# Kernel optimization log

Hardware: AMD Instinct MI355X
Metric: run time of the kernel (lower is better)

Reference implementation:

```python
import jax, jax.numpy as jnp
import numpy as np
from jax import lax

B, N, M, K = 8, 8192, 2000, 16       # batch, raw pts, subsampled pts, neighbors
C1, C2, OUT = 128, 256, 100          # backbone widths, output_embed_size


def _fps(coords, m):
    """Farthest point sampling. coords [B,N,3] -> indices [B,m] (int32)."""
    b, n, _ = coords.shape
    init_last = jnp.zeros((b,), jnp.int32)

    def body(carry, _):
        mind, last = carry
        p = jnp.take_along_axis(coords, last[:, None, None], axis=1)  # [b,1,3]
        d = jnp.sum((coords - p) ** 2, axis=-1)                        # [b,n]
        mind = jnp.minimum(mind, d)
        nxt = jnp.argmax(mind, axis=-1).astype(jnp.int32)
        return (mind, nxt), nxt

    init = (jnp.full((b, n), 1e30, coords.dtype), init_last)
    _, rest = lax.scan(body, init, None, length=m - 1)                 # [m-1,b]
    return jnp.concatenate([init_last[None], rest], axis=0).T          # [b,m]


def _gather(src, idx):
    # src [B,N,C], idx [B,...] -> [B,...,C]
    return jax.vmap(lambda s, i: s[i])(src, idx)


def _knn(q, src, k):
    # squared-distance via |q|^2+|s|^2-2q.s to avoid a [B,M,N,3] intermediate
    d2 = (jnp.sum(q * q, -1)[:, :, None]
          + jnp.sum(src * src, -1)[:, None, :]
          - 2.0 * jnp.einsum('bmd,bnd->bmn', q, src))
    return lax.top_k(-d2, k)[1]                                        # [B,M,k]


def setup_inputs() -> dict:
    key = jax.random.key(0)
    ks = jax.random.split(key, 3)
    x = jax.random.uniform(ks[0], (B, N, 3), jnp.float32)
    W1 = jax.random.normal(ks[1], (6, C1), jnp.float32) * 0.1
    b1 = jnp.zeros((C1,), jnp.float32)
    W2 = jax.random.normal(ks[2], (3 + C1, C2), jnp.float32) * 0.1
    b2 = jnp.zeros((C2,), jnp.float32)
    return {"x": x, "W1": W1, "b1": b1, "W2": W2, "b2": b2}


def reference(x, W1, b1, W2, b2):
    coords = x
    cg = lax.stop_gradient(coords)          # indices are non-differentiable
    fps_idx = _fps(cg, M)                   # [B,M]
    sub = _gather(coords, fps_idx)          # [B,M,3]
    sub_g = lax.stop_gradient(sub)

    # --- point-conv layer 1: neighbors among raw points, feats = coords ---
    idx1 = _knn(sub_g, cg, K)               # [B,M,K]
    ngh = _gather(coords, idx1)             # [B,M,K,3]
    rel1 = ngh - sub[:, :, None, :]
    h1 = jax.nn.relu(jnp.einsum('bmkf,fc->bmkc',
                                jnp.concatenate([rel1, ngh], -1), W1) + b1)
    f1 = jnp.max(h1, axis=2)                # [B,M,C1]

    # --- point-conv layer 2: neighbors among subsampled points ---
    idx2 = _knn(sub_g, sub_g, K)            # [B,M,K]
    ngh2 = _gather(sub, idx2)               # [B,M,K,3]
    rel2 = ngh2 - sub[:, :, None, :]
    fg = _gather(f1, idx2)                  # [B,M,K,C1]
    h2 = jax.nn.relu(jnp.einsum('bmkf,fc->bmkc',
                                jnp.concatenate([rel2, fg], -1), W2) + b2)
    f2 = jnp.max(h2, axis=2)                # [B,M,C2]

    # --- fused adaptive max+avg pool: M % OUT == 0 -> uniform windows ---
    feat = jnp.transpose(f2, (0, 2, 1))     # [B,C2,M]
    windows = feat.reshape(B, C2, OUT, M // OUT)
    return jnp.max(windows, axis=-1) + jnp.mean(windows, axis=-1)  # [B,C2,OUT]
```

## Files before the change

### kernel.cpp

```cpp
#include <hip/hip_runtime.h>

#define B_    8
#define N_    8192
#define M_    2000
#define K_    16
#define C1_   128
#define C2_   256
#define OUT_  100
#define SUBP_ 2048

#define FPS_T 512
#define FPS_P 16

__device__ __forceinline__ unsigned long long umax64(unsigned long long a, unsigned long long b) {
    return a > b ? a : b;
}

template<int CTRL>
__device__ __forceinline__ unsigned long long dpp_max_u64(unsigned long long v) {
    int lo = __builtin_amdgcn_update_dpp(0, (int)(unsigned)(v & 0xFFFFFFFFull), CTRL, 0xF, 0xF, true);
    int hi = __builtin_amdgcn_update_dpp(0, (int)(v >> 32),                     CTRL, 0xF, 0xF, true);
    unsigned long long o = ((unsigned long long)(unsigned)hi << 32) | (unsigned)lo;
    return umax64(v, o);
}

template<int CTRL>
__device__ __forceinline__ float dpp_min_f32(float v) {
    int o = __builtin_amdgcn_update_dpp(__float_as_int(v), __float_as_int(v), CTRL, 0xF, 0xF, false);
    return fminf(v, __int_as_float(o));
}

__device__ __forceinline__ int spread3(int v) {
    return (v & 1) | ((v & 2) << 2) | ((v & 4) << 4);
}

__global__ __launch_bounds__(FPS_T, 1) void fps_kernel(const float* __restrict__ x,
                                                       float4* __restrict__ coords4,
                                                       float4* __restrict__ sub4) {
    int b = blockIdx.x;
    int t = threadIdx.x;
    int w = t >> 6, lane = t & 63;
    const float* X = x + (size_t)b * N_ * 3;
    float4* C4 = coords4 + b * N_;

    __shared__ float4 Clds[N_];
    __shared__ unsigned short sidx[N_];
    __shared__ unsigned int hist[512];
    __shared__ __align__(16) unsigned long long wkey[2][8];

    if (t < 512) hist[t] = 0u;
    if (t < SUBP_ - M_)
        sub4[b*SUBP_ + M_ + t] = make_float4(1e15f, 1e15f, 1e15f, 3e30f);
    __syncthreads();

    int cellv[FPS_P];
#pragma unroll
    for (int j = 0; j < FPS_P; ++j) {
        int i = t + j*FPS_T;
        float xx = X[i*3+0], yy = X[i*3+1], zz = X[i*3+2];
        float ss = fmaf(zz, zz, fmaf(yy, yy, xx*xx));
        float4 p = make_float4(xx, yy, zz, ss);
        C4[i] = p;
        Clds[i] = p;
        int cx = (int)(p.x * 8.0f); cx = cx < 0 ? 0 : (cx > 7 ? 7 : cx);
        int cy = (int)(p.y * 8.0f); cy = cy < 0 ? 0 : (cy > 7 ? 7 : cy);
        int cz = (int)(p.z * 8.0f); cz = cz < 0 ? 0 : (cz > 7 ? 7 : cz);
        int cell = (spread3(cx) << 2) | (spread3(cy) << 1) | spread3(cz);
        cellv[j] = cell;
        atomicAdd(&hist[cell], 1u);
    }
    __syncthreads();

    if (w == 0) {
        unsigned loc[8], tot = 0u;
#pragma unroll
        for (int c2 = 0; c2 < 8; ++c2) { loc[c2] = hist[lane*8 + c2]; tot += loc[c2]; }
        unsigned pre = tot;
#pragma unroll
        for (int d = 1; d < 64; d <<= 1) {
            unsigned o = __shfl_up(pre, d, 64);
            if (lane >= (unsigned)d) pre += o;
        }
        unsigned run = pre - tot;
#pragma unroll
        for (int c2 = 0; c2 < 8; ++c2) { unsigned v = loc[c2]; hist[lane*8 + c2] = run; run += v; }
    }
    __syncthreads();

#pragma unroll
    for (int j = 0; j < FPS_P; ++j) {
        int i = t + j*FPS_T;
        unsigned pos = atomicAdd(&hist[cellv[j]], 1u);
        sidx[pos] = (unsigned short)i;
    }
    __syncthreads();

    int oct = (w < 4) ? w : 11 - w;
    int sbase = oct*1024 + lane*FPS_P;
    float px_[FPS_P], py_[FPS_P], pz_[FPS_P], mind[FPS_P];
    unsigned inv_[FPS_P];
    float wx0 =  1e30f, wy0 =  1e30f, wz0 =  1e30f;
    float wx1 = -1e30f, wy1 = -1e30f, wz1 = -1e30f;
#pragma unroll
    for (int j = 0; j < FPS_P; ++j) {
        int o = (int)sidx[sbase + j];
        float4 p = Clds[o];
        px_[j] = p.x; py_[j] = p.y; pz_[j] = p.z;
        mind[j] = 1e30f;
        inv_[j] = 0xFFFFFFFFu - (unsigned)o;
        wx0 = fminf(wx0, p.x); wx1 = fmaxf(wx1, p.x);
        wy0 = fminf(wy0, p.y); wy1 = fmaxf(wy1, p.y);
        wz0 = fminf(wz0, p.z); wz1 = fmaxf(wz1, p.z);
    }
    for (int s = 1; s < 64; s <<= 1) {
        wx0 = fminf(wx0, __shfl_xor(wx0, s, 64)); wx1 = fmaxf(wx1, __shfl_xor(wx1, s, 64));
        wy0 = fminf(wy0, __shfl_xor(wy0, s, 64)); wy1 = fmaxf(wy1, __shfl_xor(wy1, s, 64));
        wz0 = fminf(wz0, __shfl_xor(wz0, s, 64)); wz1 = fmaxf(wz1, __shfl_xor(wz1, s, 64));
    }

    float4 P0 = Clds[0];
    if (t == 0) sub4[b*SUBP_] = P0;
    float Px = P0.x, Py = P0.y, Pz = P0.z;
    unsigned long long wk = ((unsigned long long)__float_as_uint(1e30f) << 32);
    float wmaxf = 1e30f;

    for (int i = 1; i < M_; ++i) {
        float qx = fminf(fmaxf(Px, wx0), wx1);
        float qy = fminf(fmaxf(Py, wy0), wy1);
        float qz = fminf(fmaxf(Pz, wz0), wz1);
        float ddx = Px - qx, ddy = Py - qy, ddz = Pz - qz;
        float dmin2 = fmaf(ddz, ddz, fmaf(ddy, ddy, ddx*ddx));
        if (dmin2 * 0.99999f < wmaxf) {
            float runmax = -3.4e38f;
            unsigned ib = 0u;
#pragma unroll
            for (int j = 0; j < FPS_P; ++j) {
                float dx = px_[j] - Px, dy = py_[j] - Py, dz = pz_[j] - Pz;
                float d = fmaf(dz, dz, fmaf(dy, dy, dx*dx));
                float m = fminf(mind[j], d);
                mind[j] = m;
                ib = (m > runmax) ? inv_[j] : ib;
                runmax = fmaxf(runmax, m);
            }
            unsigned long long best = ((unsigned long long)__float_as_uint(runmax) << 32)
                                    | (unsigned long long)ib;
            best = dpp_max_u64<0x111>(best);
            best = dpp_max_u64<0x112>(best);
            best = dpp_max_u64<0x114>(best);
            best = dpp_max_u64<0x118>(best);
            best = dpp_max_u64<0x142>(best);
            best = dpp_max_u64<0x143>(best);
            wk = best;
            wmaxf = __uint_as_float((unsigned)__builtin_amdgcn_readlane((int)(unsigned)(wk >> 32), 63));
        }
        if (lane == 63) wkey[i & 1][w] = wk;
        __syncthreads();
        const ulonglong2* wk2 = (const ulonglong2*)wkey[i & 1];
        ulonglong2 q0 = wk2[0], q1 = wk2[1], q2 = wk2[2], q3 = wk2[3];
        unsigned long long gk = umax64(umax64(umax64(q0.x, q0.y), umax64(q1.x, q1.y)),
                                       umax64(umax64(q2.x, q2.y), umax64(q3.x, q3.y)));
        int last = (int)(0xFFFFFFFFu - (unsigned)(gk & 0xFFFFFFFFull));
        float4 P4 = Clds[last];
        Px = P4.x; Py = P4.y; Pz = P4.z;
        if (t == 0) sub4[b*SUBP_ + i] = P4;
    }
}

template<int NCH, int PITCH, bool TO_LDS>
__device__ __forceinline__ void knn_core(const float4* __restrict__ cand,
                                         float4 Q, int b, int base,
                                         int* __restrict__ outIdx, int* __restrict__ ldsIdx) {
    int lane = threadIdx.x & 63;
    const float4* Cb = cand + (size_t)b * PITCH;

    float v[16];
#pragma unroll
    for (int tt = 0; tt < 16; ++tt) v[tt] = 3.4e38f;

#pragma unroll 2
    for (int j = 0; j < NCH; ++j) {
        float4 c = Cb[j*64 + lane];
        float dot = fmaf(c.z, Q.z, fmaf(c.y, Q.y, c.x * Q.x));
        float d = fmaf(-2.0f, dot, Q.w + c.w);
        v[15] = fminf(v[15], d);
#pragma unroll
        for (int tt = 15; tt >= 1; --tt) {
            float lo = fminf(v[tt-1], v[tt]);
            float hi = fmaxf(v[tt-1], v[tt]);
            v[tt-1] = lo; v[tt] = hi;
        }
    }

    float T = 0.0f;
    for (int r = 0; r < 16; ++r) {
        float g = v[0];
        g = dpp_min_f32<0x111>(g);
        g = dpp_min_f32<0x112>(g);
        g = dpp_min_f32<0x114>(g);
        g = dpp_min_f32<0x118>(g);
        g = dpp_min_f32<0x142>(g);
        g = dpp_min_f32<0x143>(g);
        g = __int_as_float(__builtin_amdgcn_readlane(__float_as_int(g), 63));
        unsigned long long mk = __ballot(v[0] == g);
        int fl = __ffsll(mk) - 1;
        if (lane == fl) {
#pragma unroll
            for (int tt = 0; tt < 15; ++tt) v[tt] = v[tt+1];
            v[15] = 3.4e38f;
        }
        T = g;
    }

    unsigned long long mlt = (1ull << lane) - 1ull;
    int cnt = 0;
    for (int j = 0; j < NCH; ++j) {
        float4 c = Cb[j*64 + lane];
        float dot = fmaf(c.z, Q.z, fmaf(c.y, Q.y, c.x * Q.x));
        float d = fmaf(-2.0f, dot, Q.w + c.w);
        bool lt = d < T;
        unsigned long long m1 = __ballot(lt);
        if (lt) {
            int slot = cnt + __popcll(m1 & mlt);
            if (TO_LDS) ldsIdx[slot] = j*64 + lane; else outIdx[base + slot] = j*64 + lane;
        }
        cnt += __popcll(m1);
    }
    int rem = K_ - cnt;
    for (int j = 0; j < NCH && rem > 0; ++j) {
        float4 c = Cb[j*64 + lane];
        float dot = fmaf(c.z, Q.z, fmaf(c.y, Q.y, c.x * Q.x));
        float d = fmaf(-2.0f, dot, Q.w + c.w);
        bool eq = (d == T);
        unsigned long long m2 = __ballot(eq);
        int bef = __popcll(m2 & mlt);
        if (eq && bef < rem) {
            int slot = cnt + bef;
            if (TO_LDS) ldsIdx[slot] = j*64 + lane; else outIdx[base + slot] = j*64 + lane;
        }
        int take = __popcll(m2); if (take > rem) take = rem;
        cnt += take; rem -= take;
    }
}

__global__ __launch_bounds__(256) void knn_fused_kernel(const float4* __restrict__ coords4,
                                                        const float4* __restrict__ sub4,
                                                        int* __restrict__ idx2,
                                                        const float* __restrict__ W1,
                                                        const float* __restrict__ b1,
                                                        float* __restrict__ f1) {
    __shared__ int   nbuf[4][K_];
    __shared__ float4 nghl[4][K_];
    int blk = blockIdx.x;
    int wv = threadIdx.x >> 6, lane = threadIdx.x & 63;
    if (blk < B_*M_/4) {
        int q = blk * 4 + wv;
        int b = q / M_, m = q % M_;
        float4 Q = sub4[b * SUBP_ + m];
        knn_core<N_/64, N_, true>(coords4, Q, b, 0, nullptr, nbuf[wv]);
        __syncthreads();
        if (lane < K_) nghl[wv][lane] = coords4[(size_t)b*N_ + nbuf[wv][lane]];
        __syncthreads();
        float w0  = W1[lane],          w1  = W1[C1_ + lane],    w2  = W1[2*C1_ + lane];
        float w3  = W1[3*C1_ + lane],  w4  = W1[4*C1_ + lane],  w5  = W1[5*C1_ + lane];
        float w0b = W1[lane+64],       w1b = W1[C1_ + lane+64], w2b = W1[2*C1_ + lane+64];
        float w3b = W1[3*C1_+lane+64], w4b = W1[4*C1_+lane+64], w5b = W1[5*C1_ + lane+64];
        float bias = b1[lane], biasb = b1[lane+64];
        float mxa = -3.4e38f, mxb = -3.4e38f;
#pragma unroll
        for (int k = 0; k < K_; ++k) {
            float4 n = nghl[wv][k];
            float rx = n.x - Q.x, ry = n.y - Q.y, rz = n.z - Q.z;
            float s = rx*w0; s = fmaf(ry,w1,s); s = fmaf(rz,w2,s);
            s = fmaf(n.x,w3,s); s = fmaf(n.y,w4,s); s = fmaf(n.z,w5,s);
            s += bias; s = fmaxf(s, 0.0f); mxa = fmaxf(mxa, s);
            float sb = rx*w0b; sb = fmaf(ry,w1b,sb); sb = fmaf(rz,w2b,sb);
            sb = fmaf(n.x,w3b,sb); sb = fmaf(n.y,w4b,sb); sb = fmaf(n.z,w5b,sb);
            sb += biasb; sb = fmaxf(sb, 0.0f); mxb = fmaxf(mxb, sb);
        }
        f1[q*C1_ + lane]      = mxa;
        f1[q*C1_ + lane + 64] = mxb;
    } else {
        int q = (blk - B_*M_/4) * 4 + wv;
        int b = q / M_, m = q % M_;
        float4 Q = sub4[b * SUBP_ + m];
        knn_core<SUBP_/64, SUBP_, false>(sub4, Q, b, q*K_, idx2, nullptr);
    }
}

#define FPAD 20
typedef float v2f __attribute__((ext_vector_type(2)));
__global__ __launch_bounds__(64) void layer2_kernel(const float4* __restrict__ sub4,
        const float* __restrict__ f1, const int* __restrict__ idx2,
        const float* __restrict__ W2, const float* __restrict__ b2,
        float* __restrict__ f2) {
    int q = blockIdx.x;
    int b = q / M_, m = q % M_;
    int t = threadIdx.x;
    __shared__ __align__(16) float feat[(3 + C1_) * FPAD];
    __shared__ int nidx[K_];
    float4 Q = sub4[b*SUBP_ + m];
    if (t < K_) {
        int ik = idx2[q*K_ + t];
        nidx[t] = ik;
        float4 n = sub4[b*SUBP_ + ik];
        feat[0*FPAD + t] = n.x - Q.x;
        feat[1*FPAD + t] = n.y - Q.y;
        feat[2*FPAD + t] = n.z - Q.z;
    }
    __syncthreads();
    for (int e = t; e < K_ * C1_; e += 64) {
        int k = e >> 7, cc = e & 127;
        feat[(3 + cc)*FPAD + k] = f1[(b*M_ + nidx[k])*C1_ + cc];
    }
    __syncthreads();

    v2f acc2[K_][2];
#pragma unroll
    for (int k = 0; k < K_; ++k) { acc2[k][0] = (v2f){0.f,0.f}; acc2[k][1] = (v2f){0.f,0.f}; }
    int c0 = t * 4;
    for (int f = 0; f < 3 + C1_; ++f) {
        float4 wv = *(const float4*)(W2 + f*C2_ + c0);
        v2f w01 = (v2f){wv.x, wv.y}, w23 = (v2f){wv.z, wv.w};
        const float* row = feat + f*FPAD;
        float4 g0 = *(const float4*)(row + 0);
        float4 g1 = *(const float4*)(row + 4);
        float4 g2 = *(const float4*)(row + 8);
        float4 g3 = *(const float4*)(row + 12);
        float gk[16] = {g0.x,g0.y,g0.z,g0.w, g1.x,g1.y,g1.z,g1.w,
                        g2.x,g2.y,g2.z,g2.w, g3.x,g3.y,g3.z,g3.w};
#pragma unroll
        for (int k = 0; k < K_; ++k) {
            v2f gg = (v2f){gk[k], gk[k]};
            acc2[k][0] = __builtin_elementwise_fma(gg, w01, acc2[k][0]);
            acc2[k][1] = __builtin_elementwise_fma(gg, w23, acc2[k][1]);
        }
    }
    float4 bb = *(const float4*)(b2 + c0);
    float mx0 = -3.4e38f, mx1 = -3.4e38f, mx2 = -3.4e38f, mx3 = -3.4e38f;
#pragma unroll
    for (int k = 0; k < K_; ++k) {
        float h0 = fmaxf(acc2[k][0].x + bb.x, 0.0f);
        float h1 = fmaxf(acc2[k][0].y + bb.y, 0.0f);
        float h2 = fmaxf(acc2[k][1].x + bb.z, 0.0f);
        float h3 = fmaxf(acc2[k][1].y + bb.w, 0.0f);
        mx0 = fmaxf(mx0, h0); mx1 = fmaxf(mx1, h1);
        mx2 = fmaxf(mx2, h2); mx3 = fmaxf(mx3, h3);
    }
    *(float4*)(f2 + q*C2_ + c0) = make_float4(mx0, mx1, mx2, mx3);
}

__global__ __launch_bounds__(256) void pool_kernel(const float* __restrict__ f2,
                                                   float* __restrict__ out) {
    int bo = blockIdx.x;
    int b = bo / OUT_, o = bo % OUT_;
    int c = threadIdx.x;
    float mx = -3.4e38f, sm = 0.0f;
#pragma unroll
    for (int w = 0; w < M_/OUT_; ++w) {
        float v = f2[(b*M_ + o*(M_/OUT_) + w)*C2_ + c];
        mx = fmaxf(mx, v);
        sm += v;
    }
    out[(b*C2_ + c)*OUT_ + o] = mx + sm / (float)(M_/OUT_);
}

extern "C" void kernel_launch(void* const* d_in, const int* in_sizes, int n_in,
                              void* d_out, int out_size, void* d_ws, size_t ws_size,
                              hipStream_t stream) {
    const float* x  = (const float*)d_in[0];
    const float* W1 = (const float*)d_in[1];
    const float* b1 = (const float*)d_in[2];
    const float* W2 = (const float*)d_in[3];
    const float* b2 = (const float*)d_in[4];
    float* out = (float*)d_out;

    char* ws = (char*)d_ws;
    size_t off = 0;
    auto alloc = [&](size_t bytes) {
        void* p = ws + off;
        off += (bytes + 255) & ~(size_t)255;
        return p;
    };
    float4* coords4 = (float4*)alloc((size_t)B_*N_*sizeof(float4));
    float4* sub4    = (float4*)alloc((size_t)B_*SUBP_*sizeof(float4));
    int*    idx2    = (int*)  alloc((size_t)B_*M_*K_*sizeof(int));
    float*  f1      = (float*)alloc((size_t)B_*M_*C1_*sizeof(float));
    float*  f2      = (float*)alloc((size_t)B_*M_*C2_*sizeof(float));

    fps_kernel<<<B_, FPS_T, 0, stream>>>(x, coords4, sub4);
    knn_fused_kernel<<<2*B_*M_/4, 256, 0, stream>>>(coords4, sub4, idx2, W1, b1, f1);
    layer2_kernel<<<B_*M_, 64, 0, stream>>>(sub4, f1, idx2, W2, b2, f2);
    pool_kernel<<<B_*OUT_, 256, 0, stream>>>(f2, out);
}
```

Baseline: 1.911 ms.

## Fuse FPS and KNN into a persistent kernel with progress-flag producer/consumer overlap

```diff
diff --git a/kernel.cpp b/kernel.cpp
--- a/kernel.cpp
+++ b/kernel.cpp
@@ -8,9 +8,8 @@
 #define C2_   256
 #define OUT_  100
 #define SUBP_ 2048
-
-#define FPS_T 512
-#define FPS_P 16
+#define NCB_  248
+
 
 __device__ __forceinline__ unsigned long long umax64(unsigned long long a, unsigned long long b) {
     return a > b ? a : b;
@@ -32,138 +31,6 @@
 
 __device__ __forceinline__ int spread3(int v) {
     return (v & 1) | ((v & 2) << 2) | ((v & 4) << 4);
-}
-
-__global__ __launch_bounds__(FPS_T, 1) void fps_kernel(const float* __restrict__ x,
-                                                       float4* __restrict__ coords4,
-                                                       float4* __restrict__ sub4) {
-    int b = blockIdx.x;
-    int t = threadIdx.x;
-    int w = t >> 6, lane = t & 63;
-    const float* X = x + (size_t)b * N_ * 3;
-    float4* C4 = coords4 + b * N_;
-
-    __shared__ float4 Clds[N_];
-    __shared__ unsigned short sidx[N_];
-    __shared__ unsigned int hist[512];
-    __shared__ __align__(16) unsigned long long wkey[2][8];
-
-    if (t < 512) hist[t] = 0u;
-    if (t < SUBP_ - M_)
-        sub4[b*SUBP_ + M_ + t] = make_float4(1e15f, 1e15f, 1e15f, 3e30f);
-    __syncthreads();
-
-    int cellv[FPS_P];
-#pragma unroll
-    for (int j = 0; j < FPS_P; ++j) {
-        int i = t + j*FPS_T;
-        float xx = X[i*3+0], yy = X[i*3+1], zz = X[i*3+2];
-        float ss = fmaf(zz, zz, fmaf(yy, yy, xx*xx));
-        float4 p = make_float4(xx, yy, zz, ss);
-        C4[i] = p;
-        Clds[i] = p;
-        int cx = (int)(p.x * 8.0f); cx = cx < 0 ? 0 : (cx > 7 ? 7 : cx);
-        int cy = (int)(p.y * 8.0f); cy = cy < 0 ? 0 : (cy > 7 ? 7 : cy);
-        int cz = (int)(p.z * 8.0f); cz = cz < 0 ? 0 : (cz > 7 ? 7 : cz);
-        int cell = (spread3(cx) << 2) | (spread3(cy) << 1) | spread3(cz);
-        cellv[j] = cell;
-        atomicAdd(&hist[cell], 1u);
-    }
-    __syncthreads();
-
-    if (w == 0) {
-        unsigned loc[8], tot = 0u;
-#pragma unroll
-        for (int c2 = 0; c2 < 8; ++c2) { loc[c2] = hist[lane*8 + c2]; tot += loc[c2]; }
-        unsigned pre = tot;
-#pragma unroll
-        for (int d = 1; d < 64; d <<= 1) {
-            unsigned o = __shfl_up(pre, d, 64);
-            if (lane >= (unsigned)d) pre += o;
-        }
-        unsigned run = pre - tot;
-#pragma unroll
-        for (int c2 = 0; c2 < 8; ++c2) { unsigned v = loc[c2]; hist[lane*8 + c2] = run; run += v; }
-    }
-    __syncthreads();
-
-#pragma unroll
-    for (int j = 0; j < FPS_P; ++j) {
-        int i = t + j*FPS_T;
-        unsigned pos = atomicAdd(&hist[cellv[j]], 1u);
-        sidx[pos] = (unsigned short)i;
-    }
-    __syncthreads();
-
-    int oct = (w < 4) ? w : 11 - w;
-    int sbase = oct*1024 + lane*FPS_P;
-    float px_[FPS_P], py_[FPS_P], pz_[FPS_P], mind[FPS_P];
-    unsigned inv_[FPS_P];
-    float wx0 =  1e30f, wy0 =  1e30f, wz0 =  1e30f;
-    float wx1 = -1e30f, wy1 = -1e30f, wz1 = -1e30f;
-#pragma unroll
-    for (int j = 0; j < FPS_P; ++j) {
-        int o = (int)sidx[sbase + j];
-        float4 p = Clds[o];
-        px_[j] = p.x; py_[j] = p.y; pz_[j] = p.z;
-        mind[j] = 1e30f;
-        inv_[j] = 0xFFFFFFFFu - (unsigned)o;
-        wx0 = fminf(wx0, p.x); wx1 = fmaxf(wx1, p.x);
-        wy0 = fminf(wy0, p.y); wy1 = fmaxf(wy1, p.y);
-        wz0 = fminf(wz0, p.z); wz1 = fmaxf(wz1, p.z);
-    }
-    for (int s = 1; s < 64; s <<= 1) {
-        wx0 = fminf(wx0, __shfl_xor(wx0, s, 64)); wx1 = fmaxf(wx1, __shfl_xor(wx1, s, 64));
-        wy0 = fminf(wy0, __shfl_xor(wy0, s, 64)); wy1 = fmaxf(wy1, __shfl_xor(wy1, s, 64));
-        wz0 = fminf(wz0, __shfl_xor(wz0, s, 64)); wz1 = fmaxf(wz1, __shfl_xor(wz1, s, 64));
-    }
-
-    float4 P0 = Clds[0];
-    if (t == 0) sub4[b*SUBP_] = P0;
-    float Px = P0.x, Py = P0.y, Pz = P0.z;
-    unsigned long long wk = ((unsigned long long)__float_as_uint(1e30f) << 32);
-    float wmaxf = 1e30f;
-
-    for (int i = 1; i < M_; ++i) {
-        float qx = fminf(fmaxf(Px, wx0), wx1);
-        float qy = fminf(fmaxf(Py, wy0), wy1);
-        float qz = fminf(fmaxf(Pz, wz0), wz1);
-        float ddx = Px - qx, ddy = Py - qy, ddz = Pz - qz;
-        float dmin2 = fmaf(ddz, ddz, fmaf(ddy, ddy, ddx*ddx));
-        if (dmin2 * 0.99999f < wmaxf) {
-            float runmax = -3.4e38f;
-            unsigned ib = 0u;
-#pragma unroll
-            for (int j = 0; j < FPS_P; ++j) {
-                float dx = px_[j] - Px, dy = py_[j] - Py, dz = pz_[j] - Pz;
-                float d = fmaf(dz, dz, fmaf(dy, dy, dx*dx));
-                float m = fminf(mind[j], d);
-                mind[j] = m;
-                ib = (m > runmax) ? inv_[j] : ib;
-                runmax = fmaxf(runmax, m);
-            }
-            unsigned long long best = ((unsigned long long)__float_as_uint(runmax) << 32)
-                                    | (unsigned long long)ib;
-            best = dpp_max_u64<0x111>(best);
-            best = dpp_max_u64<0x112>(best);
-            best = dpp_max_u64<0x114>(best);
-            best = dpp_max_u64<0x118>(best);
-            best = dpp_max_u64<0x142>(best);
-            best = dpp_max_u64<0x143>(best);
-            wk = best;
-            wmaxf = __uint_as_float((unsigned)__builtin_amdgcn_readlane((int)(unsigned)(wk >> 32), 63));
-        }
-        if (lane == 63) wkey[i & 1][w] = wk;
-        __syncthreads();
-        const ulonglong2* wk2 = (const ulonglong2*)wkey[i & 1];
-        ulonglong2 q0 = wk2[0], q1 = wk2[1], q2 = wk2[2], q3 = wk2[3];
-        unsigned long long gk = umax64(umax64(umax64(q0.x, q0.y), umax64(q1.x, q1.y)),
-                                       umax64(umax64(q2.x, q2.y), umax64(q3.x, q3.y)));
-        int last = (int)(0xFFFFFFFFu - (unsigned)(gk & 0xFFFFFFFFull));
-        float4 P4 = Clds[last];
-        Px = P4.x; Py = P4.y; Pz = P4.z;
-        if (t == 0) sub4[b*SUBP_ + i] = P4;
-    }
 }
 
 template<int NCH, int PITCH, bool TO_LDS>
@@ -242,49 +109,194 @@
     }
 }
 
-__global__ __launch_bounds__(256) void knn_fused_kernel(const float4* __restrict__ coords4,
-                                                        const float4* __restrict__ sub4,
-                                                        int* __restrict__ idx2,
-                                                        const float* __restrict__ W1,
-                                                        const float* __restrict__ b1,
-                                                        float* __restrict__ f1) {
-    __shared__ int   nbuf[4][K_];
-    __shared__ float4 nghl[4][K_];
-    int blk = blockIdx.x;
-    int wv = threadIdx.x >> 6, lane = threadIdx.x & 63;
-    if (blk < B_*M_/4) {
-        int q = blk * 4 + wv;
-        int b = q / M_, m = q % M_;
-        float4 Q = sub4[b * SUBP_ + m];
-        knn_core<N_/64, N_, true>(coords4, Q, b, 0, nullptr, nbuf[wv]);
+__global__ __launch_bounds__(512, 1) void mega_kernel(const float* __restrict__ x,
+                                                      float4* __restrict__ coords4,
+                                                      float4* __restrict__ sub4,
+                                                      int* __restrict__ idx2,
+                                                      const float* __restrict__ W1,
+                                                      const float* __restrict__ b1,
+                                                      float* __restrict__ f1,
+                                                      int* __restrict__ progress) {
+    __shared__ float4 Clds[N_];
+    __shared__ unsigned short sidx[N_];
+    __shared__ unsigned int hist[512];
+    __shared__ __align__(16) unsigned long long wkey[2][8];
+    __shared__ int   nbuf[8][K_];
+    __shared__ float4 nghl[8][K_];
+
+    int t = threadIdx.x;
+    int w = t >> 6, lane = t & 63;
+
+    if (blockIdx.x < B_) {
+        int b = blockIdx.x;
+        const float* X = x + (size_t)b * N_ * 3;
+        float4* C4 = coords4 + b * N_;
+
+        if (t < 512) hist[t] = 0u;
+        if (t < SUBP_ - M_)
+            sub4[b*SUBP_ + M_ + t] = make_float4(1e15f, 1e15f, 1e15f, 3e30f);
         __syncthreads();
-        if (lane < K_) nghl[wv][lane] = coords4[(size_t)b*N_ + nbuf[wv][lane]];
+
+        int cellv[16];
+#pragma unroll
+        for (int j = 0; j < 16; ++j) {
+            int i = t + j*512;
+            float xx = X[i*3+0], yy = X[i*3+1], zz = X[i*3+2];
+            float ss = fmaf(zz, zz, fmaf(yy, yy, xx*xx));
+            float4 p = make_float4(xx, yy, zz, ss);
+            C4[i] = p;
+            Clds[i] = p;
+            int cx = (int)(p.x * 8.0f); cx = cx < 0 ? 0 : (cx > 7 ? 7 : cx);
+            int cy = (int)(p.y * 8.0f); cy = cy < 0 ? 0 : (cy > 7 ? 7 : cy);
+            int cz = (int)(p.z * 8.0f); cz = cz < 0 ? 0 : (cz > 7 ? 7 : cz);
+            int cell = (spread3(cx) << 2) | (spread3(cy) << 1) | spread3(cz);
+            cellv[j] = cell;
+            atomicAdd(&hist[cell], 1u);
+        }
         __syncthreads();
-        float w0  = W1[lane],          w1  = W1[C1_ + lane],    w2  = W1[2*C1_ + lane];
-        float w3  = W1[3*C1_ + lane],  w4  = W1[4*C1_ + lane],  w5  = W1[5*C1_ + lane];
-        float w0b = W1[lane+64],       w1b = W1[C1_ + lane+64], w2b = W1[2*C1_ + lane+64];
-        float w3b = W1[3*C1_+lane+64], w4b = W1[4*C1_+lane+64], w5b = W1[5*C1_ + lane+64];
+
+        if (w == 0) {
+            unsigned loc[8], tot = 0u;
+#pragma unroll
+            for (int c2 = 0; c2 < 8; ++c2) { loc[c2] = hist[lane*8 + c2]; tot += loc[c2]; }
+            unsigned pre = tot;
+#pragma unroll
+            for (int d = 1; d < 64; d <<= 1) {
+                unsigned o = __shfl_up(pre, d, 64);
+                if (lane >= (unsigned)d) pre += o;
+            }
+            unsigned run = pre - tot;
+#pragma unroll
+            for (int c2 = 0; c2 < 8; ++c2) { unsigned v = loc[c2]; hist[lane*8 + c2] = run; run += v; }
+        }
+        __syncthreads();
+
+#pragma unroll
+        for (int j = 0; j < 16; ++j) {
+            int i = t + j*512;
+            unsigned pos = atomicAdd(&hist[cellv[j]], 1u);
+            sidx[pos] = (unsigned short)i;
+        }
+        __syncthreads();
+
+        int oct = (w < 4) ? w : 11 - w;
+        int sbase = oct*1024 + lane*16;
+        float px_[16], py_[16], pz_[16], mind[16];
+        unsigned inv_[16];
+        float wx0 =  1e30f, wy0 =  1e30f, wz0 =  1e30f;
+        float wx1 = -1e30f, wy1 = -1e30f, wz1 = -1e30f;
+#pragma unroll
+        for (int j = 0; j < 16; ++j) {
+            int o = (int)sidx[sbase + j];
+            float4 p = Clds[o];
+            px_[j] = p.x; py_[j] = p.y; pz_[j] = p.z;
+            mind[j] = 1e30f;
+            inv_[j] = 0xFFFFFFFFu - (unsigned)o;
+            wx0 = fminf(wx0, p.x); wx1 = fmaxf(wx1, p.x);
+            wy0 = fminf(wy0, p.y); wy1 = fmaxf(wy1, p.y);
+            wz0 = fminf(wz0, p.z); wz1 = fmaxf(wz1, p.z);
+        }
+        for (int s = 1; s < 64; s <<= 1) {
+            wx0 = fminf(wx0, __shfl_xor(wx0, s, 64)); wx1 = fmaxf(wx1, __shfl_xor(wx1, s, 64));
+            wy0 = fminf(wy0, __shfl_xor(wy0, s, 64)); wy1 = fmaxf(wy1, __shfl_xor(wy1, s, 64));
+            wz0 = fminf(wz0, __shfl_xor(wz0, s, 64)); wz1 = fmaxf(wz1, __shfl_xor(wz1, s, 64));
+        }
+
+        float4 P0 = Clds[0];
+        if (t == 0) sub4[b*SUBP_] = P0;
+        float Px = P0.x, Py = P0.y, Pz = P0.z;
+        unsigned long long wk = ((unsigned long long)__float_as_uint(1e30f) << 32);
+        float wmaxf = 1e30f;
+
+        for (int i = 1; i < M_; ++i) {
+            float qx = fminf(fmaxf(Px, wx0), wx1);
+            float qy = fminf(fmaxf(Py, wy0), wy1);
+            float qz = fminf(fmaxf(Pz, wz0), wz1);
+            float ddx = Px - qx, ddy = Py - qy, ddz = Pz - qz;
+            float dmin2 = fmaf(ddz, ddz, fmaf(ddy, ddy, ddx*ddx));
+            if (dmin2 * 0.99999f < wmaxf) {
+                float runmax = -3.4e38f;
+                unsigned ib = 0u;
+#pragma unroll
+                for (int j = 0; j < 16; ++j) {
+                    float dx = px_[j] - Px, dy = py_[j] - Py, dz = pz_[j] - Pz;
+                    float d = fmaf(dz, dz, fmaf(dy, dy, dx*dx));
+                    float m = fminf(mind[j], d);
+                    mind[j] = m;
+                    ib = (m > runmax) ? inv_[j] : ib;
+                    runmax = fmaxf(runmax, m);
+                }
+                unsigned long long best = ((unsigned long long)__float_as_uint(runmax) << 32)
+                                        | (unsigned long long)ib;
+                best = dpp_max_u64<0x111>(best);
+                best = dpp_max_u64<0x112>(best);
+                best = dpp_max_u64<0x114>(best);
+                best = dpp_max_u64<0x118>(best);
+                best = dpp_max_u64<0x142>(best);
+                best = dpp_max_u64<0x143>(best);
+                wk = best;
+                wmaxf = __uint_as_float((unsigned)__builtin_amdgcn_readlane((int)(unsigned)(wk >> 32), 63));
+            }
+            if (lane == 63) wkey[i & 1][w] = wk;
+            __syncthreads();
+            const ulonglong2* wk2 = (const ulonglong2*)wkey[i & 1];
+            ulonglong2 q0 = wk2[0], q1 = wk2[1], q2 = wk2[2], q3 = wk2[3];
+            unsigned long long gk = umax64(umax64(umax64(q0.x, q0.y), umax64(q1.x, q1.y)),
+                                           umax64(umax64(q2.x, q2.y), umax64(q3.x, q3.y)));
+            int last = (int)(0xFFFFFFFFu - (unsigned)(gk & 0xFFFFFFFFull));
+            float4 P4 = Clds[last];
+            Px = P4.x; Py = P4.y; Pz = P4.z;
+            if (t == 0) {
+                sub4[b*SUBP_ + i] = P4;
+                if (((i + 1) & 31) == 0)
+                    __hip_atomic_store(&progress[b], i + 1, __ATOMIC_RELEASE, __HIP_MEMORY_SCOPE_AGENT);
+            }
+        }
+        if (t == 0)
+            __hip_atomic_store(&progress[b], M_, __ATOMIC_RELEASE, __HIP_MEMORY_SCOPE_AGENT);
+    } else {
+        int cb = blockIdx.x - B_;
+        int bb = w;
+        float w0  = W1[lane],            w1  = W1[C1_ + lane],      w2  = W1[2*C1_ + lane];
+        float w3  = W1[3*C1_ + lane],    w4  = W1[4*C1_ + lane],    w5  = W1[5*C1_ + lane];
+        float w0b = W1[lane+64],         w1b = W1[C1_ + lane+64],   w2b = W1[2*C1_ + lane+64];
+        float w3b = W1[3*C1_ + lane+64], w4b = W1[4*C1_ + lane+64], w5b = W1[5*C1_ + lane+64];
         float bias = b1[lane], biasb = b1[lane+64];
-        float mxa = -3.4e38f, mxb = -3.4e38f;
-#pragma unroll
-        for (int k = 0; k < K_; ++k) {
-            float4 n = nghl[wv][k];
-            float rx = n.x - Q.x, ry = n.y - Q.y, rz = n.z - Q.z;
-            float s = rx*w0; s = fmaf(ry,w1,s); s = fmaf(rz,w2,s);
-            s = fmaf(n.x,w3,s); s = fmaf(n.y,w4,s); s = fmaf(n.z,w5,s);
-            s += bias; s = fmaxf(s, 0.0f); mxa = fmaxf(mxa, s);
-            float sb = rx*w0b; sb = fmaf(ry,w1b,sb); sb = fmaf(rz,w2b,sb);
-            sb = fmaf(n.x,w3b,sb); sb = fmaf(n.y,w4b,sb); sb = fmaf(n.z,w5b,sb);
-            sb += biasb; sb = fmaxf(sb, 0.0f); mxb = fmaxf(mxb, sb);
-        }
-        f1[q*C1_ + lane]      = mxa;
-        f1[q*C1_ + lane + 64] = mxb;
-    } else {
-        int q = (blk - B_*M_/4) * 4 + wv;
-        int b = q / M_, m = q % M_;
-        float4 Q = sub4[b * SUBP_ + m];
-        knn_core<SUBP_/64, SUBP_, false>(sub4, Q, b, q*K_, idx2, nullptr);
-    }
+
+        for (int m = cb; m < M_; m += NCB_) {
+            while (__hip_atomic_load(&progress[bb], __ATOMIC_ACQUIRE, __HIP_MEMORY_SCOPE_AGENT) < m + 1)
+                __builtin_amdgcn_s_sleep(32);
+            float4 Q = sub4[bb*SUBP_ + m];
+            knn_core<N_/64, N_, true>(coords4, Q, bb, 0, nullptr, nbuf[w]);
+            if (lane < K_) nghl[w][lane] = coords4[(size_t)bb*N_ + nbuf[w][lane]];
+            float mxa = -3.4e38f, mxb = -3.4e38f;
+#pragma unroll
+            for (int k = 0; k < K_; ++k) {
+                float4 n = nghl[w][k];
+                float rx = n.x - Q.x, ry = n.y - Q.y, rz = n.z - Q.z;
+                float s = rx*w0; s = fmaf(ry,w1,s); s = fmaf(rz,w2,s);
+                s = fmaf(n.x,w3,s); s = fmaf(n.y,w4,s); s = fmaf(n.z,w5,s);
+                s += bias; s = fmaxf(s, 0.0f); mxa = fmaxf(mxa, s);
+                float sb = rx*w0b; sb = fmaf(ry,w1b,sb); sb = fmaf(rz,w2b,sb);
+                sb = fmaf(n.x,w3b,sb); sb = fmaf(n.y,w4b,sb); sb = fmaf(n.z,w5b,sb);
+                sb += biasb; sb = fmaxf(sb, 0.0f); mxb = fmaxf(mxb, sb);
+            }
+            int q = bb*M_ + m;
+            f1[q*C1_ + lane]      = mxa;
+            f1[q*C1_ + lane + 64] = mxb;
+        }
+        while (__hip_atomic_load(&progress[bb], __ATOMIC_ACQUIRE, __HIP_MEMORY_SCOPE_AGENT) < M_)
+            __builtin_amdgcn_s_sleep(32);
+        for (int m = cb; m < M_; m += NCB_) {
+            float4 Q = sub4[bb*SUBP_ + m];
+            int q = bb*M_ + m;
+            knn_core<SUBP_/64, SUBP_, false>(sub4, Q, bb, q*K_, idx2, nullptr);
+        }
+    }
+}
+
+__global__ void zero_kernel(int* __restrict__ p) {
+    if (threadIdx.x < B_) p[threadIdx.x] = 0;
 }
 
 #define FPAD 20
@@ -386,9 +398,10 @@
     int*    idx2    = (int*)  alloc((size_t)B_*M_*K_*sizeof(int));
     float*  f1      = (float*)alloc((size_t)B_*M_*C1_*sizeof(float));
     float*  f2      = (float*)alloc((size_t)B_*M_*C2_*sizeof(float));
-
-    fps_kernel<<<B_, FPS_T, 0, stream>>>(x, coords4, sub4);
-    knn_fused_kernel<<<2*B_*M_/4, 256, 0, stream>>>(coords4, sub4, idx2, W1, b1, f1);
+    int*    progress= (int*)  alloc((size_t)B_*sizeof(int));
+
+    zero_kernel<<<1, 64, 0, stream>>>(progress);
+    mega_kernel<<<B_ + NCB_, 512, 0, stream>>>(x, coords4, sub4, idx2, W1, b1, f1, progress);
     layer2_kernel<<<B_*M_, 64, 0, stream>>>(sub4, f1, idx2, W2, b2, f2);
     pool_kernel<<<B_*OUT_, 256, 0, stream>>>(f2, out);
 }
```

Result: slower. 1.985 ms (+3.9%).
